# Kernel tuning notes

Hardware: AMD Instinct MI355X
Metric: run time of the kernel (lower is better)

The kernel has to match this reference:

```python
import jax, jax.numpy as jnp
import numpy as np

B, G, FI, FO, H, W = 16, 8, 64, 64, 64, 64
N_ITER = 3


def setup_inputs() -> dict:
    key = jax.random.key(0)
    kx, kw, kb = jax.random.split(key, 3)
    x = jax.random.normal(kx, (B, G * FI, H, W), dtype=jnp.float32)
    # kaiming_normal_ on [fo*g, fi, 1, 1]: std = sqrt(2 / fan_in), fan_in = fi*1*1
    weight = jax.random.normal(kw, (FO * G, FI, 1, 1), dtype=jnp.float32) * np.sqrt(2.0 / FI)
    bias = jax.random.normal(kb, (1, FO, 1, 1), dtype=jnp.float32) * 0.01
    return {"x": x, "weight": weight, "bias": bias}


def reference(x, weight, bias):
    g, n_iter = G, N_ITER
    gfo, fi = weight.shape[:2]
    fo = gfo // g
    b, c, h, w = x.shape
    # grouped 1x1 conv == per-group channel matmul
    xg = x.reshape(b, g, fi, h, w)
    wg = weight.reshape(g, fo, fi)
    con = jnp.einsum('bgihw,gfi->bgfhw', xg, wg)  # [B, g, fo, H, W]
    beta = jnp.zeros((), dtype=x.dtype)
    for i in range(n_iter):
        alpha = jax.nn.sigmoid(beta)
        v = jnp.sum(alpha * con, axis=1, keepdims=True)  # [B, 1, fo, H, W]
        if i == n_iter - 1:
            out = v[:, 0]  # [B, fo, H, W]
            return out + bias
        beta = beta + jnp.sum(v * con, axis=2, keepdims=True)  # [B, g, 1, H, W]
```

## Files before the change

kernel.cpp:

```cpp
#include <hip/hip_runtime.h>


typedef __attribute__((ext_vector_type(8))) _Float16 half8;
typedef __attribute__((ext_vector_type(4))) float f32x4;

#define NG   8
#define NFI  64
#define NFO  64
#define HW   4096

__device__ __forceinline__ float sigmoidf_fast(float v) {
    float e = __builtin_amdgcn_exp2f(-1.44269504088896f * v);
    return __builtin_amdgcn_rcpf(1.0f + e);
}

__global__ __launch_bounds__(256, 2)
void routing_kernel(const float* __restrict__ x,
                    const float* __restrict__ w,
                    const float* __restrict__ bias,
                    float* __restrict__ out) {
    const int tid  = threadIdx.x;
    const int b    = blockIdx.x >> 6;
    const int p0   = (blockIdx.x & 63) << 6;
    const int lane = tid & 63;
    const int wv   = tid >> 6;
    const int pl   = lane & 15;
    const int q    = lane >> 4;
    const int pw   = wv * 16 + pl;

    __shared__ float    xlds[3][64 * 64];
    __shared__ _Float16 wlds[2][16 * 512];

    const float* xbase = x + (size_t)b * (NG * NFI) * HW;

    const float* wsrc = w + (size_t)(wv * 16 + pl) * NFI + q * 8;

#define MKXS(c) \
    const int   ch##c = wv * 16 + (c) * 4 + q; \
    const float* xs##c = xbase + (size_t)ch##c * HW + p0 + ((pl * 4 - 8 * (ch##c >> 3)) & 63);
    MKXS(0) MKXS(1) MKXS(2) MKXS(3)
#undef MKXS

    const int rb0 = q * 512 + ((pw + 8 * q) & 63);
    const int rb1 = 2048 + q * 512 + ((pw + 8 * q + 32) & 63);

    f32x4 acc[NG][4];
    #pragma unroll
    for (int g = 0; g < NG; ++g)
        #pragma unroll
        for (int t = 0; t < 4; ++t)
            acc[g][t] = (f32x4){0.f, 0.f, 0.f, 0.f};

#define CB    asm volatile("" ::: "memory")
#define BAR   __builtin_amdgcn_s_barrier()
#define SB0   __builtin_amdgcn_sched_barrier(0)
#define WAITV(N) asm volatile("s_waitcnt vmcnt(" #N ")" ::: "memory")
#define LGKM0 asm volatile("s_waitcnt lgkmcnt(0)" ::: "memory")

#define WLOAD(G, NM)                                                          \
    NM##a = *(const f32x4*)(wsrc + (size_t)(G) * 4096);                       \
    NM##b = *(const f32x4*)(wsrc + (size_t)(G) * 4096 + 4);                   \
    NM##c = *(const f32x4*)(wsrc + (size_t)(G) * 4096 + 32);                  \
    NM##d = *(const f32x4*)(wsrc + (size_t)(G) * 4096 + 36);

#define WCONV(G, NM)                                                          \
    {                                                                         \
        half8 h0_, h1_, l0_, l1_;                                             \
        _Pragma("unroll")                                                     \
        for (int j = 0; j < 4; ++j) {                                         \
            float f0 = NM##a[j], f1 = NM##b[j], f2 = NM##c[j], f3 = NM##d[j]; \
            _Float16 e0 = (_Float16)f0, e1 = (_Float16)f1;                    \
            _Float16 e2 = (_Float16)f2, e3 = (_Float16)f3;                    \
            h0_[j] = e0; h0_[j + 4] = e1;                                     \
            h1_[j] = e2; h1_[j + 4] = e3;                                     \
            l0_[j]     = (_Float16)(f0 - (float)e0);                          \
            l0_[j + 4] = (_Float16)(f1 - (float)e1);                          \
            l1_[j]     = (_Float16)(f2 - (float)e2);                          \
            l1_[j + 4] = (_Float16)(f3 - (float)e3);                          \
        }                                                                     \
        _Float16* wd_ = &wlds[(G) & 1][0] + (wv * 4) * 512 + lane * 8;        \
        *(half8*)(wd_)        = h0_;                                          \
        *(half8*)(wd_ + 512)  = h1_;                                          \
        *(half8*)(wd_ + 1024) = l0_;                                          \
        *(half8*)(wd_ + 1536) = l1_;                                          \
    }

#define XSTAGE(G, BUF)                                                        \
    {                                                                         \
        const size_t go_ = (size_t)(G) * 64 * HW;                             \
        float* xd_ = &xlds[BUF][0] + (wv * 16) * 64;                          \
        __builtin_amdgcn_global_load_lds(                                     \
            (const __attribute__((address_space(1))) void*)(xs0 + go_),       \
            (__attribute__((address_space(3))) void*)(xd_), 16, 0, 0);        \
        __builtin_amdgcn_global_load_lds(                                     \
            (const __attribute__((address_space(1))) void*)(xs1 + go_),       \
            (__attribute__((address_space(3))) void*)(xd_ + 256), 16, 0, 0);  \
        __builtin_amdgcn_global_load_lds(                                     \
            (const __attribute__((address_space(1))) void*)(xs2 + go_),       \
            (__attribute__((address_space(3))) void*)(xd_ + 512), 16, 0, 0);  \
        __builtin_amdgcn_global_load_lds(                                     \
            (const __attribute__((address_space(1))) void*)(xs3 + go_),       \
            (__attribute__((address_space(3))) void*)(xd_ + 768), 16, 0, 0);  \
    }

#define XGRP(G, BUF)                                                         \
    {                                                                        \
        const float* xr0_ = &xlds[BUF][0] + rb0;                             \
        const float* xr1_ = &xlds[BUF][0] + rb1;                             \
        half8 b0, b1;                                                        \
        b0[0] = (_Float16)xr0_[0 * 64]; b0[1] = (_Float16)xr0_[1 * 64];      \
        b0[2] = (_Float16)xr0_[2 * 64]; b0[3] = (_Float16)xr0_[3 * 64];      \
        b0[4] = (_Float16)xr0_[4 * 64]; b0[5] = (_Float16)xr0_[5 * 64];      \
        b0[6] = (_Float16)xr0_[6 * 64]; b0[7] = (_Float16)xr0_[7 * 64];      \
        b1[0] = (_Float16)xr1_[0 * 64]; b1[1] = (_Float16)xr1_[1 * 64];      \
        b1[2] = (_Float16)xr1_[2 * 64]; b1[3] = (_Float16)xr1_[3 * 64];      \
        b1[4] = (_Float16)xr1_[4 * 64]; b1[5] = (_Float16)xr1_[5 * 64];      \
        b1[6] = (_Float16)xr1_[6 * 64]; b1[7] = (_Float16)xr1_[7 * 64];      \
        const _Float16* wg_ = &wlds[(G) & 1][0] + lane * 8;                  \
        _Pragma("unroll")                                                    \
        for (int t = 0; t < 4; ++t) {                                        \
            const _Float16* wp_ = wg_ + (size_t)t * 2048;                    \
            half8 a0h = *(const half8*)(wp_);                                \
            half8 a1h = *(const half8*)(wp_ + 512);                          \
            half8 a0l = *(const half8*)(wp_ + 1024);                         \
            half8 a1l = *(const half8*)(wp_ + 1536);                         \
            acc[G][t] = __builtin_amdgcn_mfma_f32_16x16x32_f16(a0h, b0, acc[G][t], 0, 0, 0); \
            acc[G][t] = __builtin_amdgcn_mfma_f32_16x16x32_f16(a1h, b1, acc[G][t], 0, 0, 0); \
            acc[G][t] = __builtin_amdgcn_mfma_f32_16x16x32_f16(a0l, b0, acc[G][t], 0, 0, 0); \
            acc[G][t] = __builtin_amdgcn_mfma_f32_16x16x32_f16(a1l, b1, acc[G][t], 0, 0, 0); \
        }                                                                    \
    }

    f32x4 Waa, Wab, Wac, Wad;
    f32x4 Wba, Wbb, Wbc, Wbd;

    WLOAD(0, Wa) CB; XSTAGE(0, 0); CB;
    WLOAD(1, Wb) CB; XSTAGE(1, 1); CB;
    XSTAGE(2, 2); CB;

    WAITV(12); WCONV(0, Wa) LGKM0; BAR; SB0; XGRP(0, 0); BAR; WLOAD(2, Wa) CB; XSTAGE(3, 0); CB;
    WAITV(12); WCONV(1, Wb) LGKM0; BAR; SB0; XGRP(1, 1); BAR; WLOAD(3, Wb) CB; XSTAGE(4, 1); CB;
    WAITV(12); WCONV(2, Wa) LGKM0; BAR; SB0; XGRP(2, 2); BAR; WLOAD(4, Wa) CB; XSTAGE(5, 2); CB;
    WAITV(12); WCONV(3, Wb) LGKM0; BAR; SB0; XGRP(3, 0); BAR; WLOAD(5, Wb) CB; XSTAGE(6, 0); CB;
    WAITV(12); WCONV(4, Wa) LGKM0; BAR; SB0; XGRP(4, 1); BAR; WLOAD(6, Wa) CB; XSTAGE(7, 1); CB;
    WAITV(12); WCONV(5, Wb) LGKM0; BAR; SB0; XGRP(5, 2); BAR; WLOAD(7, Wb) CB;
    WAITV(8);  WCONV(6, Wa) LGKM0; BAR; SB0; XGRP(6, 0); BAR;
    WAITV(0);  WCONV(7, Wb) LGKM0; BAR; SB0; XGRP(7, 1);

#undef XGRP
#undef XSTAGE
#undef WCONV
#undef WLOAD
#undef CB
#undef BAR
#undef SB0
#undef WAITV
#undef LGKM0

    float v0[4][4];
    #pragma unroll
    for (int t = 0; t < 4; ++t)
        #pragma unroll
        for (int r = 0; r < 4; ++r) {
            float s = 0.f;
            #pragma unroll
            for (int g = 0; g < NG; ++g) s += acc[g][t][r];
            v0[t][r] = 0.5f * s;
        }

    float beta[NG], alpha[NG];
    #pragma unroll
    for (int g = 0; g < NG; ++g) {
        float s = 0.f;
        #pragma unroll
        for (int t = 0; t < 4; ++t)
            #pragma unroll
            for (int r = 0; r < 4; ++r)
                s += v0[t][r] * acc[g][t][r];
        s += __shfl_xor(s, 16);
        s += __shfl_xor(s, 32);
        beta[g]  = s;
        alpha[g] = sigmoidf_fast(s);
    }

    #pragma unroll
    for (int t = 0; t < 4; ++t)
        #pragma unroll
        for (int r = 0; r < 4; ++r) {
            float s = 0.f;
            #pragma unroll
            for (int g = 0; g < NG; ++g) s += alpha[g] * acc[g][t][r];
            v0[t][r] = s;
        }
    #pragma unroll
    for (int g = 0; g < NG; ++g) {
        float s = 0.f;
        #pragma unroll
        for (int t = 0; t < 4; ++t)
            #pragma unroll
            for (int r = 0; r < 4; ++r)
                s += v0[t][r] * acc[g][t][r];
        s += __shfl_xor(s, 16);
        s += __shfl_xor(s, 32);
        beta[g] += s;
        alpha[g] = sigmoidf_fast(beta[g]);
    }

    #pragma unroll
    for (int t = 0; t < 4; ++t)
        #pragma unroll
        for (int r = 0; r < 4; ++r) {
            int f = t * 16 + q * 4 + r;
            float s = bias[f];
            #pragma unroll
            for (int g = 0; g < NG; ++g) s += alpha[g] * acc[g][t][r];
            out[((size_t)(b * NFO + f)) * HW + p0 + pw] = s;
        }
}

extern "C" void kernel_launch(void* const* d_in, const int* in_sizes, int n_in,
                              void* d_out, int out_size, void* d_ws, size_t ws_size,
                              hipStream_t stream) {
    const float* x    = (const float*)d_in[0];
    const float* w    = (const float*)d_in[1];
    const float* bias = (const float*)d_in[2];
    float* out = (float*)d_out;
    (void)d_ws; (void)ws_size;

    routing_kernel<<<1024, 256, 0, stream>>>(x, w, bias, out);
}
```

Measured before the change: 202.1 us.

## Split output features across two wave halves with 512-thread blocks and LDS reduction

Doubles the block to 8 waves. Each pixel strip is now handled by two waves, each owning half of the output features. This halves the per-thread accumulator registers and staging loads, aiming for higher occupancy and more latency hiding. The routing dot-product reductions over output features now need a cross-wave exchange through LDS with extra block barriers. That exchange reuses an x staging buffer.

```diff
diff --git a/kernel.cpp b/kernel.cpp
--- a/kernel.cpp
+++ b/kernel.cpp
@@ -14,7 +14,7 @@
     return __builtin_amdgcn_rcpf(1.0f + e);
 }
 
-__global__ __launch_bounds__(256, 2)
+__global__ __launch_bounds__(512, 4)
 void routing_kernel(const float* __restrict__ x,
                     const float* __restrict__ w,
                     const float* __restrict__ bias,
@@ -24,32 +24,35 @@
     const int p0   = (blockIdx.x & 63) << 6;
     const int lane = tid & 63;
     const int wv   = tid >> 6;
+    const int ps   = wv & 3;
+    const int fh   = wv >> 2;
     const int pl   = lane & 15;
     const int q    = lane >> 4;
-    const int pw   = wv * 16 + pl;
+    const int pw   = ps * 16 + pl;
 
     __shared__ float    xlds[3][64 * 64];
     __shared__ _Float16 wlds[2][16 * 512];
 
     const float* xbase = x + (size_t)b * (NG * NFI) * HW;
 
-    const float* wsrc = w + (size_t)(wv * 16 + pl) * NFI + q * 8;
+    const int t_s = wv >> 1, kh = wv & 1;
+    const float* wsrc = w + (size_t)(t_s * 16 + pl) * NFI + kh * 32 + q * 8;
 
 #define MKXS(c) \
-    const int   ch##c = wv * 16 + (c) * 4 + q; \
+    const int   ch##c = wv * 8 + (c) * 4 + q; \
     const float* xs##c = xbase + (size_t)ch##c * HW + p0 + ((pl * 4 - 8 * (ch##c >> 3)) & 63);
-    MKXS(0) MKXS(1) MKXS(2) MKXS(3)
+    MKXS(0) MKXS(1)
 #undef MKXS
 
     const int rb0 = q * 512 + ((pw + 8 * q) & 63);
     const int rb1 = 2048 + q * 512 + ((pw + 8 * q + 32) & 63);
 
-    f32x4 acc[NG][4];
+    f32x4 acc[NG][2];
     #pragma unroll
     for (int g = 0; g < NG; ++g)
         #pragma unroll
-        for (int t = 0; t < 4; ++t)
-            acc[g][t] = (f32x4){0.f, 0.f, 0.f, 0.f};
+        for (int tt = 0; tt < 2; ++tt)
+            acc[g][tt] = (f32x4){0.f, 0.f, 0.f, 0.f};
 
 #define CB    asm volatile("" ::: "memory")
 #define BAR   __builtin_amdgcn_s_barrier()
@@ -59,48 +62,34 @@
 
 #define WLOAD(G, NM)                                                          \
     NM##a = *(const f32x4*)(wsrc + (size_t)(G) * 4096);                       \
-    NM##b = *(const f32x4*)(wsrc + (size_t)(G) * 4096 + 4);                   \
-    NM##c = *(const f32x4*)(wsrc + (size_t)(G) * 4096 + 32);                  \
-    NM##d = *(const f32x4*)(wsrc + (size_t)(G) * 4096 + 36);
+    NM##b = *(const f32x4*)(wsrc + (size_t)(G) * 4096 + 4);
 
 #define WCONV(G, NM)                                                          \
     {                                                                         \
-        half8 h0_, h1_, l0_, l1_;                                             \
+        half8 hh_, ll_;                                                       \
         _Pragma("unroll")                                                     \
         for (int j = 0; j < 4; ++j) {                                         \
-            float f0 = NM##a[j], f1 = NM##b[j], f2 = NM##c[j], f3 = NM##d[j]; \
+            float f0 = NM##a[j], f1 = NM##b[j];                               \
             _Float16 e0 = (_Float16)f0, e1 = (_Float16)f1;                    \
-            _Float16 e2 = (_Float16)f2, e3 = (_Float16)f3;                    \
-            h0_[j] = e0; h0_[j + 4] = e1;                                     \
-            h1_[j] = e2; h1_[j + 4] = e3;                                     \
-            l0_[j]     = (_Float16)(f0 - (float)e0);                          \
-            l0_[j + 4] = (_Float16)(f1 - (float)e1);                          \
-            l1_[j]     = (_Float16)(f2 - (float)e2);                          \
-            l1_[j + 4] = (_Float16)(f3 - (float)e3);                          \
+            hh_[j] = e0; hh_[j + 4] = e1;                                     \
+            ll_[j]     = (_Float16)(f0 - (float)e0);                          \
+            ll_[j + 4] = (_Float16)(f1 - (float)e1);                          \
         }                                                                     \
-        _Float16* wd_ = &wlds[(G) & 1][0] + (wv * 4) * 512 + lane * 8;        \
-        *(half8*)(wd_)        = h0_;                                          \
-        *(half8*)(wd_ + 512)  = h1_;                                          \
-        *(half8*)(wd_ + 1024) = l0_;                                          \
-        *(half8*)(wd_ + 1536) = l1_;                                          \
+        _Float16* wd_ = &wlds[(G) & 1][0] + (t_s * 4 + kh) * 512 + lane * 8;  \
+        *(half8*)(wd_)        = hh_;                                          \
+        *(half8*)(wd_ + 1024) = ll_;                                          \
     }
 
 #define XSTAGE(G, BUF)                                                        \
     {                                                                         \
         const size_t go_ = (size_t)(G) * 64 * HW;                             \
-        float* xd_ = &xlds[BUF][0] + (wv * 16) * 64;                          \
+        float* xd_ = &xlds[BUF][0] + (wv * 8) * 64;                           \
         __builtin_amdgcn_global_load_lds(                                     \
             (const __attribute__((address_space(1))) void*)(xs0 + go_),       \
             (__attribute__((address_space(3))) void*)(xd_), 16, 0, 0);        \
         __builtin_amdgcn_global_load_lds(                                     \
             (const __attribute__((address_space(1))) void*)(xs1 + go_),       \
             (__attribute__((address_space(3))) void*)(xd_ + 256), 16, 0, 0);  \
-        __builtin_amdgcn_global_load_lds(                                     \
-            (const __attribute__((address_space(1))) void*)(xs2 + go_),       \
-            (__attribute__((address_space(3))) void*)(xd_ + 512), 16, 0, 0);  \
-        __builtin_amdgcn_global_load_lds(                                     \
-            (const __attribute__((address_space(1))) void*)(xs3 + go_),       \
-            (__attribute__((address_space(3))) void*)(xd_ + 768), 16, 0, 0);  \
     }
 
 #define XGRP(G, BUF)                                                         \
@@ -118,34 +107,34 @@
         b1[6] = (_Float16)xr1_[6 * 64]; b1[7] = (_Float16)xr1_[7 * 64];      \
         const _Float16* wg_ = &wlds[(G) & 1][0] + lane * 8;                  \
         _Pragma("unroll")                                                    \
-        for (int t = 0; t < 4; ++t) {                                        \
-            const _Float16* wp_ = wg_ + (size_t)t * 2048;                    \
+        for (int tt = 0; tt < 2; ++tt) {                                     \
+            const _Float16* wp_ = wg_ + (size_t)(fh * 2 + tt) * 2048;        \
             half8 a0h = *(const half8*)(wp_);                                \
             half8 a1h = *(const half8*)(wp_ + 512);                          \
             half8 a0l = *(const half8*)(wp_ + 1024);                         \
             half8 a1l = *(const half8*)(wp_ + 1536);                         \
-            acc[G][t] = __builtin_amdgcn_mfma_f32_16x16x32_f16(a0h, b0, acc[G][t], 0, 0, 0); \
-            acc[G][t] = __builtin_amdgcn_mfma_f32_16x16x32_f16(a1h, b1, acc[G][t], 0, 0, 0); \
-            acc[G][t] = __builtin_amdgcn_mfma_f32_16x16x32_f16(a0l, b0, acc[G][t], 0, 0, 0); \
-            acc[G][t] = __builtin_amdgcn_mfma_f32_16x16x32_f16(a1l, b1, acc[G][t], 0, 0, 0); \
+            acc[G][tt] = __builtin_amdgcn_mfma_f32_16x16x32_f16(a0h, b0, acc[G][tt], 0, 0, 0); \
+            acc[G][tt] = __builtin_amdgcn_mfma_f32_16x16x32_f16(a1h, b1, acc[G][tt], 0, 0, 0); \
+            acc[G][tt] = __builtin_amdgcn_mfma_f32_16x16x32_f16(a0l, b0, acc[G][tt], 0, 0, 0); \
+            acc[G][tt] = __builtin_amdgcn_mfma_f32_16x16x32_f16(a1l, b1, acc[G][tt], 0, 0, 0); \
         }                                                                    \
     }
 
-    f32x4 Waa, Wab, Wac, Wad;
-    f32x4 Wba, Wbb, Wbc, Wbd;
+    f32x4 Waa, Wab;
+    f32x4 Wba, Wbb;
 
     WLOAD(0, Wa) CB; XSTAGE(0, 0); CB;
     WLOAD(1, Wb) CB; XSTAGE(1, 1); CB;
     XSTAGE(2, 2); CB;
 
-    WAITV(12); WCONV(0, Wa) LGKM0; BAR; SB0; XGRP(0, 0); BAR; WLOAD(2, Wa) CB; XSTAGE(3, 0); CB;
-    WAITV(12); WCONV(1, Wb) LGKM0; BAR; SB0; XGRP(1, 1); BAR; WLOAD(3, Wb) CB; XSTAGE(4, 1); CB;
-    WAITV(12); WCONV(2, Wa) LGKM0; BAR; SB0; XGRP(2, 2); BAR; WLOAD(4, Wa) CB; XSTAGE(5, 2); CB;
-    WAITV(12); WCONV(3, Wb) LGKM0; BAR; SB0; XGRP(3, 0); BAR; WLOAD(5, Wb) CB; XSTAGE(6, 0); CB;
-    WAITV(12); WCONV(4, Wa) LGKM0; BAR; SB0; XGRP(4, 1); BAR; WLOAD(6, Wa) CB; XSTAGE(7, 1); CB;
-    WAITV(12); WCONV(5, Wb) LGKM0; BAR; SB0; XGRP(5, 2); BAR; WLOAD(7, Wb) CB;
-    WAITV(8);  WCONV(6, Wa) LGKM0; BAR; SB0; XGRP(6, 0); BAR;
-    WAITV(0);  WCONV(7, Wb) LGKM0; BAR; SB0; XGRP(7, 1);
+    WAITV(6); WCONV(0, Wa) LGKM0; BAR; SB0; XGRP(0, 0); BAR; WLOAD(2, Wa) CB; XSTAGE(3, 0); CB;
+    WAITV(6); WCONV(1, Wb) LGKM0; BAR; SB0; XGRP(1, 1); BAR; WLOAD(3, Wb) CB; XSTAGE(4, 1); CB;
+    WAITV(6); WCONV(2, Wa) LGKM0; BAR; SB0; XGRP(2, 2); BAR; WLOAD(4, Wa) CB; XSTAGE(5, 2); CB;
+    WAITV(6); WCONV(3, Wb) LGKM0; BAR; SB0; XGRP(3, 0); BAR; WLOAD(5, Wb) CB; XSTAGE(6, 0); CB;
+    WAITV(6); WCONV(4, Wa) LGKM0; BAR; SB0; XGRP(4, 1); BAR; WLOAD(6, Wa) CB; XSTAGE(7, 1); CB;
+    WAITV(6); WCONV(5, Wb) LGKM0; BAR; SB0; XGRP(5, 2); BAR; WLOAD(7, Wb) CB;
+    WAITV(4); WCONV(6, Wa) LGKM0; BAR; SB0; XGRP(6, 0); BAR;
+    WAITV(0); WCONV(7, Wb) LGKM0; BAR; SB0; XGRP(7, 1);
 
 #undef XGRP
 #undef XSTAGE
@@ -157,63 +146,87 @@
 #undef WAITV
 #undef LGKM0
 
-    float v0[4][4];
-    #pragma unroll
-    for (int t = 0; t < 4; ++t)
+    float* bex = (float*)&xlds[2][0];
+
+    float v0[2][4];
+    #pragma unroll
+    for (int tt = 0; tt < 2; ++tt)
         #pragma unroll
         for (int r = 0; r < 4; ++r) {
             float s = 0.f;
             #pragma unroll
-            for (int g = 0; g < NG; ++g) s += acc[g][t][r];
-            v0[t][r] = 0.5f * s;
+            for (int g = 0; g < NG; ++g) s += acc[g][tt][r];
+            v0[tt][r] = 0.5f * s;
         }
 
-    float beta[NG], alpha[NG];
+    float sg[NG];
     #pragma unroll
     for (int g = 0; g < NG; ++g) {
         float s = 0.f;
         #pragma unroll
-        for (int t = 0; t < 4; ++t)
+        for (int tt = 0; tt < 2; ++tt)
             #pragma unroll
             for (int r = 0; r < 4; ++r)
-                s += v0[t][r] * acc[g][t][r];
+                s += v0[tt][r] * acc[g][tt][r];
         s += __shfl_xor(s, 16);
         s += __shfl_xor(s, 32);
+        sg[g] = s;
+    }
+    if (q == 0) {
+        #pragma unroll
+        for (int g = 0; g < NG; ++g) bex[wv * 128 + g * 16 + pl] = sg[g];
+    }
+    __syncthreads();
+    float beta[NG], alpha[NG];
+    #pragma unroll
+    for (int g = 0; g < NG; ++g) {
+        float s = sg[g] + bex[(wv ^ 4) * 128 + g * 16 + pl];
         beta[g]  = s;
         alpha[g] = sigmoidf_fast(s);
     }
 
     #pragma unroll
-    for (int t = 0; t < 4; ++t)
+    for (int tt = 0; tt < 2; ++tt)
         #pragma unroll
         for (int r = 0; r < 4; ++r) {
             float s = 0.f;
             #pragma unroll
-            for (int g = 0; g < NG; ++g) s += alpha[g] * acc[g][t][r];
-            v0[t][r] = s;
+            for (int g = 0; g < NG; ++g) s += alpha[g] * acc[g][tt][r];
+            v0[tt][r] = s;
         }
     #pragma unroll
     for (int g = 0; g < NG; ++g) {
         float s = 0.f;
         #pragma unroll
-        for (int t = 0; t < 4; ++t)
+        for (int tt = 0; tt < 2; ++tt)
             #pragma unroll
             for (int r = 0; r < 4; ++r)
-                s += v0[t][r] * acc[g][t][r];
+                s += v0[tt][r] * acc[g][tt][r];
         s += __shfl_xor(s, 16);
         s += __shfl_xor(s, 32);
+        sg[g] = s;
+    }
+    __syncthreads();
+    if (q == 0) {
+        #pragma unroll
+        for (int g = 0; g < NG; ++g) bex[wv * 128 + g * 16 + pl] = sg[g];
+    }
+    __syncthreads();
+    #pragma unroll
+    for (int g = 0; g < NG; ++g) {
+        float s = sg[g] + bex[(wv ^ 4) * 128 + g * 16 + pl];
         beta[g] += s;
         alpha[g] = sigmoidf_fast(beta[g]);
     }
 
     #pragma unroll
-    for (int t = 0; t < 4; ++t)
+    for (int tt = 0; tt < 2; ++tt)
         #pragma unroll
         for (int r = 0; r < 4; ++r) {
-            int f = t * 16 + q * 4 + r;
+            int f = (fh * 2 + tt) * 16 + q * 4 + r;
             float s = bias[f];
             #pragma unroll
-            for (int g = 0; g < NG; ++g) s += alpha[g] * acc[g][t][r];
+            for (int g = 0; g < NG; ++g) s += alpha[g] * acc[g][tt][r];
             out[((size_t)(b * NFO + f)) * HW + p0 + pw] = s;
         }
 }
@@ -227,5 +240,5 @@
     float* out = (float*)d_out;
     (void)d_ws; (void)ws_size;
 
-    routing_kernel<<<1024, 256, 0, stream>>>(x, w, bias, out);
+    routing_kernel<<<1024, 512, 0, stream>>>(x, w, bias, out);
 }
```

Result: no change. 204.3 us (+1.1%).
